# Kernel tuning notes

Hardware: AMD Instinct MI355X
Metric: run time of the kernel (lower is better)

## Reference

```python
import jax, jax.numpy as jnp
import numpy as np

N_HEAD = 16
HEAD_DIM = 128

def rotate_half(x):
    x1, x2 = jnp.split(x, 2, axis=-1)
    return jnp.concatenate((-x2, x1), axis=-1)

def setup_inputs() -> dict:
    key = jax.random.key(0)
    ks = jax.random.split(key, 5)
    B, T, C = 2, 2048, 2048
    x = jax.random.normal(ks[0], (B, T, C), dtype=jnp.float32)
    # rotary tables as used by the module: cos/sin of shape [T, head_dim]
    pos = jnp.arange(T, dtype=jnp.float32)[:, None]
    inv_freq = 1.0 / (10000.0 ** (jnp.arange(0, HEAD_DIM, 2, dtype=jnp.float32) / HEAD_DIM))
    freqs = pos * inv_freq[None, :]            # [T, head_dim/2]
    emb = jnp.concatenate([freqs, freqs], -1)  # [T, head_dim]
    cos = jnp.cos(emb)
    sin = jnp.sin(emb)
    W_qkv = jax.random.normal(ks[1], (C, 3 * C), dtype=jnp.float32) * (C ** -0.5)
    W_proj = jax.random.normal(ks[2], (C, C), dtype=jnp.float32) * (C ** -0.5)
    return {"x": x, "cos": cos, "sin": sin, "W_qkv": W_qkv, "W_proj": W_proj}

def reference(x, cos, sin, W_qkv, W_proj):
    B, T, C = x.shape
    H, D = N_HEAD, HEAD_DIM
    qkv = x @ W_qkv                                   # [B,T,3C]
    q, k, v = jnp.split(qkv, 3, axis=2)
    # [B,T,C] -> [B,H,T,D]
    q = q.reshape(B, T, H, D).transpose(0, 2, 1, 3)
    k = k.reshape(B, T, H, D).transpose(0, 2, 1, 3)
    v = v.reshape(B, T, H, D).transpose(0, 2, 1, 3)
    c = cos[None, None, :, :]                          # [1,1,T,D]
    s = sin[None, None, :, :]
    q = q * c + rotate_half(q) * s
    k = k * c + rotate_half(k) * s
    scale = 1.0 / jnp.sqrt(jnp.float32(D))
    scores = jnp.einsum('bhqd,bhkd->bhqk', q, k) * scale
    attn = jax.nn.softmax(scores, axis=-1)
    y = jnp.einsum('bhqk,bhkd->bhqd', attn, v)         # [B,H,T,D]
    y = y.transpose(0, 2, 1, 3).reshape(B, T, C)
    return y @ W_proj
```

## Files before the change

### kernel.cpp

```cpp
#include <hip/hip_runtime.h>
#include <cstdint>
#include <cstddef>

typedef __bf16 bf16_t;
typedef __bf16 bf16x8 __attribute__((ext_vector_type(8)));
typedef __bf16 bf16x4 __attribute__((ext_vector_type(4)));
typedef float f32x4 __attribute__((ext_vector_type(4)));

#define MFMA16(a, b, c) __builtin_amdgcn_mfma_f32_16x16x32_bf16(a, b, c, 0, 0, 0)

__device__ __forceinline__ void gll16(const bf16_t* g, bf16_t* l) {
  __builtin_amdgcn_global_load_lds(
      (__attribute__((address_space(1))) uint32_t*)((uintptr_t)g),
      (__attribute__((address_space(3))) uint32_t*)((uint32_t)(uintptr_t)l),
      16, 0, 0);
}

__global__ void fill_diag(uint32_t* out, int n_u32) {
  int i = blockIdx.x * 256 + threadIdx.x;
  if (i < n_u32) out[i] = 0x447A0000u;
}

__global__ void conv_vec_f32(const float* __restrict__ in, bf16_t* __restrict__ out,
                             int n8) {
  const int i = blockIdx.x * 256 + threadIdx.x;
  if (i >= n8) return;
  const float* p = in + (size_t)i * 8;
  const f32x4 a = *(const f32x4*)p;
  const f32x4 b = *(const f32x4*)(p + 4);
  bf16x8 o;
#pragma unroll
  for (int j = 0; j < 4; ++j) {
    o[j] = (bf16_t)a[j];
    o[4 + j] = (bf16_t)b[j];
  }
  ((bf16x8*)out)[i] = o;
}

__global__ __launch_bounds__(256) void conv_transpose_f32(
    const float* __restrict__ in, bf16_t* __restrict__ out, int R, int C) {
  __shared__ bf16_t tile[64][72];
  const int bc = blockIdx.x * 64;
  const int br = blockIdx.y * 64;
  const int t = threadIdx.x;
  const int r = t >> 3;
  const int c8 = (t & 7) * 8;
#pragma unroll
  for (int ii = 0; ii < 2; ++ii) {
    const int rr = r + ii * 32;
    const float* p = in + (size_t)(br + rr) * C + bc + c8;
    const f32x4 a = *(const f32x4*)p;
    const f32x4 b = *(const f32x4*)(p + 4);
    bf16x8 v;
#pragma unroll
    for (int j = 0; j < 4; ++j) {
      v[j] = (bf16_t)a[j];
      v[4 + j] = (bf16_t)b[j];
    }
    *(bf16x8*)(&tile[rr][c8]) = v;
  }
  __syncthreads();
#pragma unroll
  for (int ii = 0; ii < 2; ++ii) {
    const int rr = r + ii * 32;
    bf16x8 o;
#pragma unroll
    for (int jj = 0; jj < 8; ++jj) o[jj] = tile[c8 + jj][rr];
    *(bf16x8*)(out + (size_t)(bc + rr) * R + br + c8) = o;
  }
}

#define MF8(MLO, AARR, BARR, NLO)                                              \
  do {                                                                         \
    _Pragma("unroll") for (int k_ = 0; k_ < 2; ++k_) {                         \
      _Pragma("unroll") for (int m_ = 0; m_ < 4; ++m_) {                       \
        _Pragma("unroll") for (int n_ = 0; n_ < 2; ++n_) {                     \
          acc[(MLO) + m_][(NLO) + n_] = MFMA16(AARR[m_][k_], BARR[n_][k_],     \
                                               acc[(MLO) + m_][(NLO) + n_]);   \
        }                                                                      \
      }                                                                        \
    }                                                                          \
  } while (0)

template <bool C32>
__global__ __launch_bounds__(512, 2) void gemm8(
    const bf16_t* __restrict__ A, const bf16_t* __restrict__ Bt,
    void* __restrict__ C, int M, int N, int K, int nbn) {
  __shared__ __align__(1024) bf16_t lds8[65536];
  bf16_t* As = lds8;
  bf16_t* Bs = lds8 + 32768;

  const int tid = threadIdx.x;
  const int lane = tid & 63;
  const int wave = tid >> 6;
  const int wr = wave >> 2;
  const int wc = wave & 3;
  const int fr = lane & 15;
  const int fg = lane >> 4;

  const int nwg = gridDim.x;
  const int bid = blockIdx.x;
  const int swz = (bid & 7) * (nwg >> 3) + (bid >> 3);
  const int m0 = (swz / nbn) * 256;
  const int n0 = (swz % nbn) * 256;

  const int NT = K >> 6;

  const int sseg0 = wave * 2;
  const int srow = lane >> 3;
  const int sj = lane & 7;

  auto stage = [&](const bf16_t* __restrict__ G, int row0, bf16_t* L, int kt,
                   int h) {
#pragma unroll
    for (int l = 0; l < 2; ++l) {
      const int seg = sseg0 + l;
      const int r = seg * 8 + srow;
      const int j = sj ^ (r & 7);
      const bf16_t* src = G + (size_t)(row0 + h * 128 + r) * K + kt * 64 + j * 8;
      gll16(src, L + ((2 * kt + h) & 3) * 8192 + seg * 512 + lane * 8);
    }
  };

  const int cb0 = (fg * 16) ^ ((fr & 7) << 4);

  auto lda = [&](bf16x8(&af)[4][2], int kt, int mlo) {
    const char* base = (const char*)(As + ((2 * kt + wr) & 3) * 8192);
#pragma unroll
    for (int m = 0; m < 4; ++m) {
      const char* p = base + ((mlo + m) * 16 + fr) * 128;
      af[m][0] = *(const bf16x8*)(p + cb0);
      af[m][1] = *(const bf16x8*)(p + (cb0 ^ 64));
    }
  };
  auto ldb = [&](bf16x8(&bf)[2][2], int kt, int nlo) {
    const char* base = (const char*)(Bs + ((2 * kt + (wc >> 1)) & 3) * 8192);
#pragma unroll
    for (int n = 0; n < 2; ++n) {
      const char* p = base + ((wc & 1) * 64 + (nlo + n) * 16 + fr) * 128;
      bf[n][0] = *(const bf16x8*)(p + cb0);
      bf[n][1] = *(const bf16x8*)(p + (cb0 ^ 64));
    }
  };

  f32x4 acc[8][4] = {};

  stage(A, m0, As, 0, 0);
  stage(A, m0, As, 0, 1);
  stage(Bt, n0, Bs, 0, 0);
  stage(Bt, n0, Bs, 0, 1);
  stage(Bt, n0, Bs, 1, 0);
  stage(Bt, n0, Bs, 1, 1);
  asm volatile("s_waitcnt vmcnt(4)" ::: "memory");
  __builtin_amdgcn_s_barrier();

  bf16x8 af[4][2], bfA[2][2], bfB[2][2];

  for (int u = 0; u < NT; u += 2) {
    const bool st2 = (u + 2 < NT);
    const bool st3 = (u + 3 < NT);
    lda(af, u, 0);
    ldb(bfA, u, 0);
    stage(A, m0, As, u + 1, 0);
    asm volatile("s_waitcnt lgkmcnt(8)" ::: "memory");
    __builtin_amdgcn_s_barrier();
    asm volatile("s_waitcnt lgkmcnt(0)" ::: "memory");
    __builtin_amdgcn_sched_barrier(0);
    __builtin_amdgcn_s_setprio(1);
    MF8(0, af, bfA, 0);
    __builtin_amdgcn_s_setprio(0);
    __builtin_amdgcn_s_barrier();
    ldb(bfB, u, 2);
    stage(A, m0, As, u + 1, 1);
    __builtin_amdgcn_s_barrier();
    asm volatile("s_waitcnt lgkmcnt(0)" ::: "memory");
    __builtin_amdgcn_sched_barrier(0);
    __builtin_amdgcn_s_setprio(1);
    MF8(0, af, bfB, 2);
    __builtin_amdgcn_s_setprio(0);
    __builtin_amdgcn_s_barrier();
    lda(af, u, 4);
    if (st2) stage(Bt, n0, Bs, u + 2, 0);
    __builtin_amdgcn_s_barrier();
    asm volatile("s_waitcnt lgkmcnt(0)" ::: "memory");
    __builtin_amdgcn_sched_barrier(0);
    __builtin_amdgcn_s_setprio(1);
    MF8(4, af, bfB, 2);
    __builtin_amdgcn_s_setprio(0);
    __builtin_amdgcn_s_barrier();
    if (st2) stage(Bt, n0, Bs, u + 2, 1);
    __builtin_amdgcn_s_barrier();
    __builtin_amdgcn_s_setprio(1);
    MF8(4, af, bfA, 0);
    __builtin_amdgcn_s_setprio(0);
    asm volatile("s_waitcnt vmcnt(4)" ::: "memory");
    __builtin_amdgcn_s_barrier();
    lda(af, u + 1, 0);
    ldb(bfA, u + 1, 0);
    if (st2) stage(A, m0, As, u + 2, 0);
    asm volatile("s_waitcnt lgkmcnt(8)" ::: "memory");
    __builtin_amdgcn_s_barrier();
    asm volatile("s_waitcnt lgkmcnt(0)" ::: "memory");
    __builtin_amdgcn_sched_barrier(0);
    __builtin_amdgcn_s_setprio(1);
    MF8(0, af, bfA, 0);
    __builtin_amdgcn_s_setprio(0);
    __builtin_amdgcn_s_barrier();
    ldb(bfB, u + 1, 2);
    if (st2) stage(A, m0, As, u + 2, 1);
    __builtin_amdgcn_s_barrier();
    asm volatile("s_waitcnt lgkmcnt(0)" ::: "memory");
    __builtin_amdgcn_sched_barrier(0);
    __builtin_amdgcn_s_setprio(1);
    MF8(0, af, bfB, 2);
    __builtin_amdgcn_s_setprio(0);
    __builtin_amdgcn_s_barrier();
    lda(af, u + 1, 4);
    if (st3) stage(Bt, n0, Bs, u + 3, 0);
    __builtin_amdgcn_s_barrier();
    asm volatile("s_waitcnt lgkmcnt(0)" ::: "memory");
    __builtin_amdgcn_sched_barrier(0);
    __builtin_amdgcn_s_setprio(1);
    MF8(4, af, bfB, 2);
    __builtin_amdgcn_s_setprio(0);
    __builtin_amdgcn_s_barrier();
    if (st3) stage(Bt, n0, Bs, u + 3, 1);
    __builtin_amdgcn_s_barrier();
    __builtin_amdgcn_s_setprio(1);
    MF8(4, af, bfA, 0);
    __builtin_amdgcn_s_setprio(0);
    asm volatile("s_waitcnt vmcnt(4)" ::: "memory");
    __builtin_amdgcn_s_barrier();
  }

#pragma unroll
  for (int m = 0; m < 8; ++m) {
#pragma unroll
    for (int n = 0; n < 4; ++n) {
#pragma unroll
      for (int r = 0; r < 4; ++r) {
        const int row = m0 + wr * 128 + m * 16 + fg * 4 + r;
        const int col = n0 + wc * 64 + n * 16 + fr;
        const size_t idx = (size_t)row * N + col;
        if (C32)
          ((float*)C)[idx] = acc[m][n][r];
        else
          ((bf16_t*)C)[idx] = (bf16_t)acc[m][n][r];
      }
    }
  }
  (void)M;
}

template <bool C32>
__global__ __launch_bounds__(256) void gemm_lds(
    const bf16_t* __restrict__ A, const bf16_t* __restrict__ Bt,
    void* __restrict__ C, int M, int N, int K) {
  __shared__ __align__(16) bf16_t As[128 * 32];
  __shared__ __align__(16) bf16_t Bs[128 * 32];
  const int tid = threadIdx.x;
  const int lane = tid & 63;
  const int wave = tid >> 6;
  const int m0 = blockIdx.x * 128;
  const int n0 = blockIdx.y * 128;
  const int wm = (wave & 1) * 64;
  const int wn = (wave >> 1) * 64;
  const int fr = lane & 15;
  const int fk = (lane >> 4) * 8;

  f32x4 acc[4][4] = {};

  const bf16_t* ga = A + (size_t)(m0 + (tid >> 2)) * K + (tid & 3) * 8;
  const bf16_t* gb = Bt + (size_t)(n0 + (tid >> 2)) * K + (tid & 3) * 8;
  bf16_t* lA = As + tid * 8;
  bf16_t* lB = Bs + tid * 8;
  const size_t half = (size_t)64 * K;

  for (int k0 = 0; k0 < K; k0 += 32) {
    __syncthreads();
    gll16(ga, lA);
    gll16(ga + half, lA + 2048);
    gll16(gb, lB);
    gll16(gb + half, lB + 2048);
    ga += 32;
    gb += 32;
    __syncthreads();
    bf16x8 af[4], bfr[4];
#pragma unroll
    for (int i = 0; i < 4; ++i)
      af[i] = *(const bf16x8*)(As + (wm + i * 16 + fr) * 32 + fk);
#pragma unroll
    for (int j = 0; j < 4; ++j)
      bfr[j] = *(const bf16x8*)(Bs + (wn + j * 16 + fr) * 32 + fk);
#pragma unroll
    for (int i = 0; i < 4; ++i)
#pragma unroll
      for (int j = 0; j < 4; ++j)
        acc[i][j] = MFMA16(af[i], bfr[j], acc[i][j]);
  }

  const int fg = lane >> 4;
#pragma unroll
  for (int i = 0; i < 4; ++i) {
#pragma unroll
    for (int j = 0; j < 4; ++j) {
#pragma unroll
      for (int r = 0; r < 4; ++r) {
        const int row = m0 + wm + i * 16 + fg * 4 + r;
        const int col = n0 + wn + j * 16 + fr;
        const size_t idx = (size_t)row * N + col;
        if (C32)
          ((float*)C)[idx] = acc[i][j][r];
        else
          ((bf16_t*)C)[idx] = (bf16_t)acc[i][j][r];
      }
    }
  }
}

template <bool A32, bool C32>
__global__ __launch_bounds__(256) void gemm_t(
    const void* __restrict__ A, const bf16_t* __restrict__ Bt,
    void* __restrict__ C, int M, int N, int K) {
  __shared__ bf16_t As[128 * 32];
  __shared__ bf16_t Bs[128 * 32];
  const int tid = threadIdx.x;
  const int lane = tid & 63;
  const int wave = tid >> 6;
  const int m0 = blockIdx.x * 128;
  const int n0 = blockIdx.y * 128;
  const int wm = (wave & 1) * 64;
  const int wn = (wave >> 1) * 64;
  const int fr = lane & 15;
  const int fk = (lane >> 4) * 8;

  f32x4 acc[4][4] = {};

  const size_t ea0 = (size_t)(m0 + (tid >> 2)) * K + (tid & 3) * 8;
  const bf16_t* gb = Bt + (size_t)(n0 + (tid >> 2)) * K + (tid & 3) * 8;
  bf16_t* lA = As + tid * 8;
  bf16_t* lB = Bs + tid * 8;
  const size_t half = (size_t)64 * K;

  for (int k0 = 0; k0 < K; k0 += 32) {
    bf16x8 ra0, ra1;
    if (A32) {
      const float* pa = (const float*)A + ea0 + k0;
      const f32x4 x0 = *(const f32x4*)pa;
      const f32x4 x1 = *(const f32x4*)(pa + 4);
      const f32x4 x2 = *(const f32x4*)(pa + half);
      const f32x4 x3 = *(const f32x4*)(pa + half + 4);
#pragma unroll
      for (int j = 0; j < 4; ++j) {
        ra0[j] = (bf16_t)x0[j];
        ra0[4 + j] = (bf16_t)x1[j];
        ra1[j] = (bf16_t)x2[j];
        ra1[4 + j] = (bf16_t)x3[j];
      }
    } else {
      const bf16_t* pa = (const bf16_t*)A + ea0 + k0;
      ra0 = *(const bf16x8*)pa;
      ra1 = *(const bf16x8*)(pa + half);
    }
    const bf16x8 rb0 = *(const bf16x8*)gb;
    const bf16x8 rb1 = *(const bf16x8*)(gb + half);
    gb += 32;
    __syncthreads();
    *(bf16x8*)lA = ra0;
    *(bf16x8*)(lA + 2048) = ra1;
    *(bf16x8*)lB = rb0;
    *(bf16x8*)(lB + 2048) = rb1;
    __syncthreads();
    bf16x8 af[4], bfr[4];
#pragma unroll
    for (int i = 0; i < 4; ++i)
      af[i] = *(const bf16x8*)(As + (wm + i * 16 + fr) * 32 + fk);
#pragma unroll
    for (int j = 0; j < 4; ++j)
      bfr[j] = *(const bf16x8*)(Bs + (wn + j * 16 + fr) * 32 + fk);
#pragma unroll
    for (int i = 0; i < 4; ++i)
#pragma unroll
      for (int j = 0; j < 4; ++j)
        acc[i][j] = MFMA16(af[i], bfr[j], acc[i][j]);
  }

  const int fg = lane >> 4;
#pragma unroll
  for (int i = 0; i < 4; ++i) {
#pragma unroll
    for (int j = 0; j < 4; ++j) {
#pragma unroll
      for (int r = 0; r < 4; ++r) {
        const int row = m0 + wm + i * 16 + fg * 4 + r;
        const int col = n0 + wn + j * 16 + fr;
        const size_t idx = (size_t)row * N + col;
        if (C32)
          ((float*)C)[idx] = acc[i][j][r];
        else
          ((bf16_t*)C)[idx] = (bf16_t)acc[i][j][r];
      }
    }
  }
}

__global__ __launch_bounds__(256) void rope_k(
    const bf16_t* __restrict__ qkv, const bf16_t* __restrict__ cosb,
    const bf16_t* __restrict__ sinb, bf16_t* __restrict__ Kr) {
  const int row = blockIdx.x;
  const int t = row & 2047;
  const int b = row >> 11;
  const int idx = threadIdx.x * 8;
  const int h = idx >> 7;
  const int d = idx & 127;
  const float sgn = (d < 64) ? -1.f : 1.f;
  const bf16_t* base = qkv + (size_t)row * 6144 + 2048;
  const bf16x8 kv = *(const bf16x8*)(base + idx);
  const bf16x8 kp = *(const bf16x8*)(base + (idx ^ 64));
  const bf16x8 cv = *(const bf16x8*)(cosb + t * 128 + d);
  const bf16x8 sv = *(const bf16x8*)(sinb + t * 128 + d);
  bf16x8 o;
#pragma unroll
  for (int jj = 0; jj < 8; ++jj)
    o[jj] = (bf16_t)(((float)kv[jj]) * ((float)cv[jj]) +
                     sgn * ((float)kp[jj]) * ((float)sv[jj]));
  *(bf16x8*)(Kr + ((size_t)(b * 16 + h) * 2048 + t) * 128 + d) = o;
}

__global__ __launch_bounds__(256) void transpose_v(
    const bf16_t* __restrict__ qkv, bf16_t* __restrict__ Vt) {
  __shared__ bf16_t tile[64][72];
  const int bh = blockIdx.z;
  const int b = bh >> 4, h = bh & 15;
  const int t0 = blockIdx.x * 64;
  const int d0 = blockIdx.y * 64;
  const int t = threadIdx.x;
  const int r = t >> 3;
  const int c8 = (t & 7) * 8;
#pragma unroll
  for (int ii = 0; ii < 2; ++ii) {
    const int rr = r + ii * 32;
    *(bf16x8*)(&tile[rr][c8]) =
        *(const bf16x8*)(qkv + (size_t)(b * 2048 + t0 + rr) * 6144 + 4096 + h * 128 + d0 + c8);
  }
  __syncthreads();
#pragma unroll
  for (int ii = 0; ii < 2; ++ii) {
    const int rr = r + ii * 32;
    bf16x8 o;
#pragma unroll
    for (int jj = 0; jj < 8; ++jj) o[jj] = tile[c8 + jj][rr];
    *(bf16x8*)(Vt + ((size_t)bh * 128 + d0 + rr) * 2048 + t0 + c8) = o;
  }
}

__global__ __launch_bounds__(256, 4) void flash_q64p(
    const bf16_t* __restrict__ qkv, const bf16_t* __restrict__ cosb,
    const bf16_t* __restrict__ sinb, const bf16_t* __restrict__ Kr,
    const bf16_t* __restrict__ Vt, bf16_t* __restrict__ Y) {
  constexpr int T = 2048;
  __shared__ __align__(1024) bf16_t Ks[64 * 128];
  __shared__ bf16_t Vs[128][72];
  const int tid = threadIdx.x;
  const int lane = tid & 63;
  const int fr = lane & 15;
  const int fg = lane >> 4;
  const int qt = blockIdx.x;
  const int bh = blockIdx.y;
  const int b = bh >> 4, h = bh & 15;

  const int wave = tid >> 6;
  const int trow = qt * 64 + wave * 16 + fr;
  const bf16_t* qrow = qkv + (size_t)(b * T + trow) * 6144 + h * 128;
  bf16x8 qf[4];
#pragma unroll
  for (int ks = 0; ks < 4; ++ks) {
    const int d = ks * 32 + fg * 8;
    const float sgn = (d < 64) ? -1.f : 1.f;
    const bf16x8 qv = *(const bf16x8*)(qrow + d);
    const bf16x8 qp = *(const bf16x8*)(qrow + (d ^ 64));
    const bf16x8 cv = *(const bf16x8*)(cosb + trow * 128 + d);
    const bf16x8 sv = *(const bf16x8*)(sinb + trow * 128 + d);
    bf16x8 o;
#pragma unroll
    for (int jj = 0; jj < 8; ++jj)
      o[jj] = (bf16_t)((((float)qv[jj]) * ((float)cv[jj]) +
                        sgn * ((float)qp[jj]) * ((float)sv[jj])) *
                       0.1275174825f);
    qf[ks] = o;
  }

  f32x4 acc[8] = {};
  float l_i = 0.f;

  const int krow = tid >> 4;
  const int sc = (tid & 15) ^ (krow & 7);
  const int vrow = tid >> 3;
  const int vu = tid & 7;
  const int vc0 = ((vu >> 2) * 32) + ((vu & 1) * 16) + (((vu >> 1) & 1) * 4);
  const bf16_t* Kh = Kr + (size_t)bh * T * 128;
  const bf16_t* Vh = Vt + (size_t)bh * 128 * T;

  auto stageK = [&](int t0) {
#pragma unroll
    for (int it = 0; it < 4; ++it)
      gll16(Kh + (size_t)(t0 + it * 16 + krow) * 128 + sc * 8,
            Ks + it * 2048 + tid * 8);
  };
  bf16x8 vreg[4];
  auto loadV = [&](int t0) {
#pragma unroll
    for (int it = 0; it < 4; ++it)
      vreg[it] = *(const bf16x8*)(Vh + (size_t)(it * 32 + vrow) * T + t0 + vu * 8);
  };
  auto writeV = [&]() {
#pragma unroll
    for (int it = 0; it < 4; ++it) {
      const int row = it * 32 + vrow;
      const bf16x8 v = vreg[it];
      bf16x4 lo, hi;
#pragma unroll
      for (int jj = 0; jj < 4; ++jj) {
        lo[jj] = v[jj];
        hi[jj] = v[4 + jj];
      }
      *(bf16x4*)(&Vs[row][vc0]) = lo;
      *(bf16x4*)(&Vs[row][vc0 + 8]) = hi;
    }
  };

  stageK(0);
  loadV(0);
  asm volatile("s_waitcnt vmcnt(0)" ::: "memory");
  __builtin_amdgcn_sched_barrier(0);
  writeV();
  __syncthreads();

  const int cswz = (fr & 7) << 4;
  const char* kbase = (const char*)Ks;

  for (int j = 0; j < T / 64; ++j) {
    f32x4 sacc[4] = {};
#pragma unroll
    for (int ks = 0; ks < 4; ++ks) {
#pragma unroll
      for (int n = 0; n < 4; ++n) {
        const bf16x8 kf = *(const bf16x8*)(kbase + (n * 16 + fr) * 256 +
                                           ((ks * 64 + fg * 16) ^ cswz));
        sacc[n] = MFMA16(kf, qf[ks], sacc[n]);
      }
    }
    __syncthreads();

    const bool more = (j + 1 < T / 64);
    if (more) {
      stageK((j + 1) * 64);
      loadV((j + 1) * 64);
    }

    bf16x8 paf[2];
    float lsum = 0.f;
#pragma unroll
    for (int ks2 = 0; ks2 < 2; ++ks2) {
#pragma unroll
      for (int jj = 0; jj < 8; ++jj) {
        const float p = exp2f(sacc[ks2 * 2 + (jj >> 2)][jj & 3]);
        lsum += p;
        paf[ks2][jj] = (bf16_t)p;
      }
    }
    l_i += lsum;

#pragma unroll
    for (int ks2 = 0; ks2 < 2; ++ks2) {
#pragma unroll
      for (int n = 0; n < 8; ++n) {
        const bf16x8 vf = *(const bf16x8*)(&Vs[n * 16 + fr][ks2 * 32 + fg * 8]);
        acc[n] = MFMA16(paf[ks2], vf, acc[n]);
      }
    }

    asm volatile("s_waitcnt vmcnt(0)" ::: "memory");
    __builtin_amdgcn_sched_barrier(0);
    __syncthreads();
    if (more) {
      writeV();
      __syncthreads();
    }
  }

  float l = l_i;
  l += __shfl_xor(l, 16, 64);
  l += __shfl_xor(l, 32, 64);
#pragma unroll
  for (int r = 0; r < 4; ++r) {
    const float inv = 1.0f / __shfl(l, fg * 4 + r, 64);
    const int t = qt * 64 + wave * 16 + fg * 4 + r;
    bf16_t* yrow = Y + (size_t)(b * T + t) * 2048 + h * 128;
#pragma unroll
    for (int n = 0; n < 8; ++n)
      yrow[n * 16 + fr] = (bf16_t)(acc[n][r] * inv);
  }
}

__global__ __launch_bounds__(256) void flash_fused_v2(
    const bf16_t* __restrict__ qkv, const bf16_t* __restrict__ cosb,
    const bf16_t* __restrict__ sinb, bf16_t* __restrict__ Y) {
  constexpr int T = 2048;
  __shared__ bf16_t Ks[64][136];
  __shared__ bf16_t Vs[128][72];
  __shared__ bf16_t Ps[128][72];
  const int tid = threadIdx.x;
  const int lane = tid & 63;
  const int wave = tid >> 6;
  const int fr = lane & 15;
  const int fg = lane >> 4;
  const int qt = blockIdx.x;
  const int bh = blockIdx.y;
  const int b = bh >> 4, h = bh & 15;

  const bf16_t* qbase = qkv + (size_t)b * T * 6144 + h * 128;
  bf16x8 qf[2][4];
#pragma unroll
  for (int i = 0; i < 2; ++i) {
    const int trow = qt * 128 + wave * 32 + i * 16 + fr;
    const bf16_t* qrow = qbase + (size_t)trow * 6144;
#pragma unroll
    for (int ks = 0; ks < 4; ++ks) {
      const int d = ks * 32 + fg * 8;
      const float sgn = (d < 64) ? -1.f : 1.f;
      const bf16x8 qv = *(const bf16x8*)(qrow + d);
      const bf16x8 qp = *(const bf16x8*)(qrow + (d ^ 64));
      const bf16x8 cv = *(const bf16x8*)(cosb + trow * 128 + d);
      const bf16x8 sv = *(const bf16x8*)(sinb + trow * 128 + d);
      bf16x8 o;
#pragma unroll
      for (int jj = 0; jj < 8; ++jj)
        o[jj] = (bf16_t)((((float)qv[jj]) * ((float)cv[jj]) +
                          sgn * ((float)qp[jj]) * ((float)sv[jj])) *
                         0.08838834764831845f);
      qf[i][ks] = o;
    }
  }

  f32x4 acc[2][8] = {};
  float l_i[2][4] = {};

  const int kr = tid >> 4;
  const int kc = (tid & 15) * 8;
  const float sgnk = (kc < 64) ? -1.f : 1.f;
  const int tp = tid & 63;

  for (int j = 0; j < T / 64; ++j) {
    const int t0 = j * 64;
#pragma unroll
    for (int it = 0; it < 4; ++it) {
      const int row = it * 16 + kr;
      const int tg = t0 + row;
      const bf16_t* krow = qkv + ((size_t)(b * T + tg)) * 6144 + 2048 + h * 128;
      const bf16x8 kv = *(const bf16x8*)(krow + kc);
      const bf16x8 kp = *(const bf16x8*)(krow + (kc ^ 64));
      const bf16x8 cv = *(const bf16x8*)(cosb + tg * 128 + kc);
      const bf16x8 sv = *(const bf16x8*)(sinb + tg * 128 + kc);
      bf16x8 o;
#pragma unroll
      for (int jj = 0; jj < 8; ++jj)
        o[jj] = (bf16_t)(((float)kv[jj]) * ((float)cv[jj]) +
                         sgnk * ((float)kp[jj]) * ((float)sv[jj]));
      *(bf16x8*)(&Ks[row][kc]) = o;
    }
#pragma unroll
    for (int cc = 0; cc < 4; ++cc) {
      const int d8 = (cc * 4 + (tid >> 6)) * 8;
      const bf16x8 vv = *(const bf16x8*)(qkv + ((size_t)(b * T + t0 + tp)) * 6144 +
                                         4096 + h * 128 + d8);
#pragma unroll
      for (int jj = 0; jj < 8; ++jj) Vs[d8 + jj][tp] = vv[jj];
    }
    __syncthreads();

    f32x4 sacc[2][4] = {};
#pragma unroll
    for (int ks = 0; ks < 4; ++ks) {
#pragma unroll
      for (int n = 0; n < 4; ++n) {
        const bf16x8 kf = *(const bf16x8*)(&Ks[n * 16 + fr][ks * 32 + fg * 8]);
        sacc[0][n] = MFMA16(qf[0][ks], kf, sacc[0][n]);
        sacc[1][n] = MFMA16(qf[1][ks], kf, sacc[1][n]);
      }
    }

#pragma unroll
    for (int i = 0; i < 2; ++i) {
#pragma unroll
      for (int r = 0; r < 4; ++r) {
        const float p0 = __expf(sacc[i][0][r]);
        const float p1 = __expf(sacc[i][1][r]);
        const float p2 = __expf(sacc[i][2][r]);
        const float p3 = __expf(sacc[i][3][r]);
        l_i[i][r] += (p0 + p1) + (p2 + p3);
        const int prow = wave * 32 + i * 16 + fg * 4 + r;
        Ps[prow][0 + fr] = (bf16_t)p0;
        Ps[prow][16 + fr] = (bf16_t)p1;
        Ps[prow][32 + fr] = (bf16_t)p2;
        Ps[prow][48 + fr] = (bf16_t)p3;
      }
    }

#pragma unroll
    for (int ks = 0; ks < 2; ++ks) {
      const bf16x8 pf0 = *(const bf16x8*)(&Ps[wave * 32 + fr][ks * 32 + fg * 8]);
      const bf16x8 pf1 = *(const bf16x8*)(&Ps[wave * 32 + 16 + fr][ks * 32 + fg * 8]);
#pragma unroll
      for (int n = 0; n < 8; ++n) {
        const bf16x8 vf = *(const bf16x8*)(&Vs[n * 16 + fr][ks * 32 + fg * 8]);
        acc[0][n] = MFMA16(pf0, vf, acc[0][n]);
        acc[1][n] = MFMA16(pf1, vf, acc[1][n]);
      }
    }
    __syncthreads();
  }

#pragma unroll
  for (int i = 0; i < 2; ++i) {
#pragma unroll
    for (int r = 0; r < 4; ++r) {
      float l = l_i[i][r];
#pragma unroll
      for (int msk = 1; msk < 16; msk <<= 1) l += __shfl_xor(l, msk, 64);
      const float inv = 1.0f / l;
      const int t = qt * 128 + wave * 32 + i * 16 + fg * 4 + r;
      bf16_t* yrow = Y + (size_t)(b * T + t) * 2048 + h * 128;
#pragma unroll
      for (int n = 0; n < 8; ++n)
        yrow[n * 16 + fr] = (bf16_t)(acc[i][n][r] * inv);
    }
  }
}

extern "C" void kernel_launch(void* const* d_in, const int* in_sizes, int n_in,
                              void* d_out, int out_size, void* d_ws, size_t ws_size,
                              hipStream_t stream) {
  const float* x = (const float*)d_in[0];
  const float* cosi = (const float*)d_in[1];
  const float* sini = (const float*)d_in[2];
  const float* Wqkv = (const float*)d_in[3];
  const float* Wproj = (const float*)d_in[4];

  const size_t NEED_FAST = sizeof(bf16_t) *
      ((size_t)12582912 + 262144 + 262144 + 25165824 + 8388608 + 8388608);
  const size_t NEED_BASE = 256 + sizeof(bf16_t) *
      ((size_t)12582912 + 4194304 + 262144 + 262144 + 25165824);

  if (ws_size >= NEED_FAST) {
    bf16_t* base = (bf16_t*)d_ws;
    bf16_t* WqkvT = base;
    bf16_t* y = base;
    bf16_t* cosb = base + 12582912;
    bf16_t* sinb = cosb + 262144;
    bf16_t* qkv = sinb + 262144;
    bf16_t* WprojT = qkv;
    bf16_t* Kr = qkv + 25165824;
    bf16_t* xb = Kr;
    bf16_t* Vt = Kr + 8388608;

    conv_vec_f32<<<128, 256, 0, stream>>>(cosi, cosb, 32768);
    conv_vec_f32<<<128, 256, 0, stream>>>(sini, sinb, 32768);
    conv_vec_f32<<<4096, 256, 0, stream>>>(x, xb, 1048576);
    conv_transpose_f32<<<dim3(96, 32), 256, 0, stream>>>(Wqkv, WqkvT, 2048, 6144);
    gemm8<false><<<384, 512, 0, stream>>>(xb, WqkvT, qkv, 4096, 6144, 2048, 24);
    rope_k<<<4096, 256, 0, stream>>>(qkv, cosb, sinb, Kr);
    transpose_v<<<dim3(32, 2, 32), 256, 0, stream>>>(qkv, Vt);
    flash_q64p<<<dim3(32, 32), 256, 0, stream>>>(qkv, cosb, sinb, Kr, Vt, y);
    conv_transpose_f32<<<dim3(32, 32), 256, 0, stream>>>(Wproj, WprojT, 2048, 2048);
    gemm_lds<true><<<dim3(32, 16), 256, 0, stream>>>(y, WprojT, d_out, 4096, 2048, 2048);
  } else if (ws_size >= NEED_BASE) {
    bf16_t* base = (bf16_t*)((char*)d_ws + 256);
    bf16_t* WqkvT = base;
    bf16_t* y = base;
    bf16_t* WprojT = base + 12582912;
    bf16_t* cosb = WprojT + 4194304;
    bf16_t* sinb = cosb + 262144;
    bf16_t* qkv = sinb + 262144;

    conv_vec_f32<<<128, 256, 0, stream>>>(cosi, cosb, 32768);
    conv_vec_f32<<<128, 256, 0, stream>>>(sini, sinb, 32768);
    conv_transpose_f32<<<dim3(96, 32), 256, 0, stream>>>(Wqkv, WqkvT, 2048, 6144);
    gemm_t<true, false><<<dim3(32, 48), 256, 0, stream>>>(x, WqkvT, qkv, 4096, 6144, 2048);
    flash_fused_v2<<<dim3(16, 32), 256, 0, stream>>>(qkv, cosb, sinb, y);
    conv_transpose_f32<<<dim3(32, 32), 256, 0, stream>>>(Wproj, WprojT, 2048, 2048);
    gemm_t<false, true><<<dim3(32, 16), 256, 0, stream>>>(y, WprojT, d_out, 4096, 2048, 2048);
  } else {
    fill_diag<<<(out_size + 255) / 256, 256, 0, stream>>>((uint32_t*)d_out, out_size);
  }
}
```

Baseline: 424.2 us.

## Switch GEMMs to 128x256 tile kernel with triple/quintuple-buffered LDS pipeline

```diff
diff --git a/kernel.cpp b/kernel.cpp
--- a/kernel.cpp
+++ b/kernel.cpp
@@ -70,25 +70,13 @@
   }
 }
 
-#define MF8(MLO, AARR, BARR, NLO)                                              \
-  do {                                                                         \
-    _Pragma("unroll") for (int k_ = 0; k_ < 2; ++k_) {                         \
-      _Pragma("unroll") for (int m_ = 0; m_ < 4; ++m_) {                       \
-        _Pragma("unroll") for (int n_ = 0; n_ < 2; ++n_) {                     \
-          acc[(MLO) + m_][(NLO) + n_] = MFMA16(AARR[m_][k_], BARR[n_][k_],     \
-                                               acc[(MLO) + m_][(NLO) + n_]);   \
-        }                                                                      \
-      }                                                                        \
-    }                                                                          \
-  } while (0)
-
 template <bool C32>
-__global__ __launch_bounds__(512, 2) void gemm8(
+__global__ __launch_bounds__(512, 2) void gemm8n(
     const bf16_t* __restrict__ A, const bf16_t* __restrict__ Bt,
     void* __restrict__ C, int M, int N, int K, int nbn) {
   __shared__ __align__(1024) bf16_t lds8[65536];
   bf16_t* As = lds8;
-  bf16_t* Bs = lds8 + 32768;
+  bf16_t* Bs = lds8 + 24576;
 
   const int tid = threadIdx.x;
   const int lane = tid & 63;
@@ -101,40 +89,38 @@
   const int nwg = gridDim.x;
   const int bid = blockIdx.x;
   const int swz = (bid & 7) * (nwg >> 3) + (bid >> 3);
-  const int m0 = (swz / nbn) * 256;
+  const int m0 = (swz / nbn) * 128;
   const int n0 = (swz % nbn) * 256;
 
   const int NT = K >> 6;
 
-  const int sseg0 = wave * 2;
-  const int srow = lane >> 3;
-  const int sj = lane & 7;
-
-  auto stage = [&](const bf16_t* __restrict__ G, int row0, bf16_t* L, int kt,
-                   int h) {
+  const int srow = tid >> 3;
+  const int sj = tid & 7;
+
+  auto stage = [&](const bf16_t* __restrict__ G, int grow0, bf16_t* slotBase,
+                   int kt) {
 #pragma unroll
     for (int l = 0; l < 2; ++l) {
-      const int seg = sseg0 + l;
-      const int r = seg * 8 + srow;
+      const int r = l * 64 + srow;
       const int j = sj ^ (r & 7);
-      const bf16_t* src = G + (size_t)(row0 + h * 128 + r) * K + kt * 64 + j * 8;
-      gll16(src, L + ((2 * kt + h) & 3) * 8192 + seg * 512 + lane * 8);
+      gll16(G + (size_t)(grow0 + r) * K + kt * 64 + j * 8,
+            slotBase + l * 4096 + tid * 8);
     }
   };
 
   const int cb0 = (fg * 16) ^ ((fr & 7) << 4);
 
-  auto lda = [&](bf16x8(&af)[4][2], int kt, int mlo) {
-    const char* base = (const char*)(As + ((2 * kt + wr) & 3) * 8192);
+  auto lda = [&](bf16x8(&af)[4][2], int t) {
+    const char* base = (const char*)(As + (t % 3) * 8192);
 #pragma unroll
     for (int m = 0; m < 4; ++m) {
-      const char* p = base + ((mlo + m) * 16 + fr) * 128;
+      const char* p = base + (wr * 64 + m * 16 + fr) * 128;
       af[m][0] = *(const bf16x8*)(p + cb0);
       af[m][1] = *(const bf16x8*)(p + (cb0 ^ 64));
     }
   };
-  auto ldb = [&](bf16x8(&bf)[2][2], int kt, int nlo) {
-    const char* base = (const char*)(Bs + ((2 * kt + (wc >> 1)) & 3) * 8192);
+  auto ldb2 = [&](bf16x8(&bf)[2][2], int t, int nlo) {
+    const char* base = (const char*)(Bs + ((2 * t + (wc >> 1)) % 5) * 8192);
 #pragma unroll
     for (int n = 0; n < 2; ++n) {
       const char* p = base + ((wc & 1) * 64 + (nlo + n) * 16 + fr) * 128;
@@ -143,103 +129,66 @@
     }
   };
 
-  f32x4 acc[8][4] = {};
-
-  stage(A, m0, As, 0, 0);
-  stage(A, m0, As, 0, 1);
-  stage(Bt, n0, Bs, 0, 0);
-  stage(Bt, n0, Bs, 0, 1);
-  stage(Bt, n0, Bs, 1, 0);
-  stage(Bt, n0, Bs, 1, 1);
-  asm volatile("s_waitcnt vmcnt(4)" ::: "memory");
+  f32x4 acc[4][4] = {};
+
+  stage(A, m0, As, 0);
+  stage(A, m0, As + 8192, 1);
+  stage(Bt, n0, Bs, 0);
+  stage(Bt, n0 + 128, Bs + 8192, 0);
+  stage(Bt, n0, Bs + 2 * 8192, 1);
+  asm volatile("s_waitcnt vmcnt(2)" ::: "memory");
   __builtin_amdgcn_s_barrier();
 
-  bf16x8 af[4][2], bfA[2][2], bfB[2][2];
-
-  for (int u = 0; u < NT; u += 2) {
-    const bool st2 = (u + 2 < NT);
-    const bool st3 = (u + 3 < NT);
-    lda(af, u, 0);
-    ldb(bfA, u, 0);
-    stage(A, m0, As, u + 1, 0);
+  bf16x8 af[4][2], bf01[2][2], bf23[2][2];
+
+  for (int t = 0; t < NT; ++t) {
+    lda(af, t);
+    ldb2(bf01, t, 0);
+    if (t + 2 < NT) stage(Bt, n0, Bs + ((2 * t + 4) % 5) * 8192, t + 2);
+    if (t + 1 < NT) stage(Bt, n0 + 128, Bs + ((2 * t + 3) % 5) * 8192, t + 1);
     asm volatile("s_waitcnt lgkmcnt(8)" ::: "memory");
     __builtin_amdgcn_s_barrier();
     asm volatile("s_waitcnt lgkmcnt(0)" ::: "memory");
     __builtin_amdgcn_sched_barrier(0);
     __builtin_amdgcn_s_setprio(1);
-    MF8(0, af, bfA, 0);
+#pragma unroll
+    for (int k = 0; k < 2; ++k)
+#pragma unroll
+      for (int m = 0; m < 4; ++m)
+#pragma unroll
+        for (int n = 0; n < 2; ++n)
+          acc[m][n] = MFMA16(af[m][k], bf01[n][k], acc[m][n]);
     __builtin_amdgcn_s_setprio(0);
     __builtin_amdgcn_s_barrier();
-    ldb(bfB, u, 2);
-    stage(A, m0, As, u + 1, 1);
+    ldb2(bf23, t, 2);
+    if (t + 2 < NT) stage(A, m0, As + ((t + 2) % 3) * 8192, t + 2);
     __builtin_amdgcn_s_barrier();
     asm volatile("s_waitcnt lgkmcnt(0)" ::: "memory");
     __builtin_amdgcn_sched_barrier(0);
     __builtin_amdgcn_s_setprio(1);
-    MF8(0, af, bfB, 2);
+#pragma unroll
+    for (int k = 0; k < 2; ++k)
+#pragma unroll
+      for (int m = 0; m < 4; ++m)
+#pragma unroll
+        for (int n = 0; n < 2; ++n)
+          acc[m][n + 2] = MFMA16(af[m][k], bf23[n][k], acc[m][n + 2]);
     __builtin_amdgcn_s_setprio(0);
+    if (t + 3 < NT) {
+      asm volatile("s_waitcnt vmcnt(2)" ::: "memory");
+    } else {
+      asm volatile("s_waitcnt vmcnt(0)" ::: "memory");
+    }
     __builtin_amdgcn_s_barrier();
-    lda(af, u, 4);
-    if (st2) stage(Bt, n0, Bs, u + 2, 0);
-    __builtin_amdgcn_s_barrier();
-    asm volatile("s_waitcnt lgkmcnt(0)" ::: "memory");
-    __builtin_amdgcn_sched_barrier(0);
-    __builtin_amdgcn_s_setprio(1);
-    MF8(4, af, bfB, 2);
-    __builtin_amdgcn_s_setprio(0);
-    __builtin_amdgcn_s_barrier();
-    if (st2) stage(Bt, n0, Bs, u + 2, 1);
-    __builtin_amdgcn_s_barrier();
-    __builtin_amdgcn_s_setprio(1);
-    MF8(4, af, bfA, 0);
-    __builtin_amdgcn_s_setprio(0);
-    asm volatile("s_waitcnt vmcnt(4)" ::: "memory");
-    __builtin_amdgcn_s_barrier();
-    lda(af, u + 1, 0);
-    ldb(bfA, u + 1, 0);
-    if (st2) stage(A, m0, As, u + 2, 0);
-    asm volatile("s_waitcnt lgkmcnt(8)" ::: "memory");
-    __builtin_amdgcn_s_barrier();
-    asm volatile("s_waitcnt lgkmcnt(0)" ::: "memory");
-    __builtin_amdgcn_sched_barrier(0);
-    __builtin_amdgcn_s_setprio(1);
-    MF8(0, af, bfA, 0);
-    __builtin_amdgcn_s_setprio(0);
-    __builtin_amdgcn_s_barrier();
-    ldb(bfB, u + 1, 2);
-    if (st2) stage(A, m0, As, u + 2, 1);
-    __builtin_amdgcn_s_barrier();
-    asm volatile("s_waitcnt lgkmcnt(0)" ::: "memory");
-    __builtin_amdgcn_sched_barrier(0);
-    __builtin_amdgcn_s_setprio(1);
-    MF8(0, af, bfB, 2);
-    __builtin_amdgcn_s_setprio(0);
-    __builtin_amdgcn_s_barrier();
-    lda(af, u + 1, 4);
-    if (st3) stage(Bt, n0, Bs, u + 3, 0);
-    __builtin_amdgcn_s_barrier();
-    asm volatile("s_waitcnt lgkmcnt(0)" ::: "memory");
-    __builtin_amdgcn_sched_barrier(0);
-    __builtin_amdgcn_s_setprio(1);
-    MF8(4, af, bfB, 2);
-    __builtin_amdgcn_s_setprio(0);
-    __builtin_amdgcn_s_barrier();
-    if (st3) stage(Bt, n0, Bs, u + 3, 1);
-    __builtin_amdgcn_s_barrier();
-    __builtin_amdgcn_s_setprio(1);
-    MF8(4, af, bfA, 0);
-    __builtin_amdgcn_s_setprio(0);
-    asm volatile("s_waitcnt vmcnt(4)" ::: "memory");
-    __builtin_amdgcn_s_barrier();
-  }
-
-#pragma unroll
-  for (int m = 0; m < 8; ++m) {
+  }
+
+#pragma unroll
+  for (int m = 0; m < 4; ++m) {
 #pragma unroll
     for (int n = 0; n < 4; ++n) {
 #pragma unroll
       for (int r = 0; r < 4; ++r) {
-        const int row = m0 + wr * 128 + m * 16 + fg * 4 + r;
+        const int row = m0 + wr * 64 + m * 16 + fg * 4 + r;
         const int col = n0 + wc * 64 + n * 16 + fr;
         const size_t idx = (size_t)row * N + col;
         if (C32)
@@ -250,72 +199,6 @@
     }
   }
   (void)M;
-}
-
-template <bool C32>
-__global__ __launch_bounds__(256) void gemm_lds(
-    const bf16_t* __restrict__ A, const bf16_t* __restrict__ Bt,
-    void* __restrict__ C, int M, int N, int K) {
-  __shared__ __align__(16) bf16_t As[128 * 32];
-  __shared__ __align__(16) bf16_t Bs[128 * 32];
-  const int tid = threadIdx.x;
-  const int lane = tid & 63;
-  const int wave = tid >> 6;
-  const int m0 = blockIdx.x * 128;
-  const int n0 = blockIdx.y * 128;
-  const int wm = (wave & 1) * 64;
-  const int wn = (wave >> 1) * 64;
-  const int fr = lane & 15;
-  const int fk = (lane >> 4) * 8;
-
-  f32x4 acc[4][4] = {};
-
-  const bf16_t* ga = A + (size_t)(m0 + (tid >> 2)) * K + (tid & 3) * 8;
-  const bf16_t* gb = Bt + (size_t)(n0 + (tid >> 2)) * K + (tid & 3) * 8;
-  bf16_t* lA = As + tid * 8;
-  bf16_t* lB = Bs + tid * 8;
-  const size_t half = (size_t)64 * K;
-
-  for (int k0 = 0; k0 < K; k0 += 32) {
-    __syncthreads();
-    gll16(ga, lA);
-    gll16(ga + half, lA + 2048);
-    gll16(gb, lB);
-    gll16(gb + half, lB + 2048);
-    ga += 32;
-    gb += 32;
-    __syncthreads();
-    bf16x8 af[4], bfr[4];
-#pragma unroll
-    for (int i = 0; i < 4; ++i)
-      af[i] = *(const bf16x8*)(As + (wm + i * 16 + fr) * 32 + fk);
-#pragma unroll
-    for (int j = 0; j < 4; ++j)
-      bfr[j] = *(const bf16x8*)(Bs + (wn + j * 16 + fr) * 32 + fk);
-#pragma unroll
-    for (int i = 0; i < 4; ++i)
-#pragma unroll
-      for (int j = 0; j < 4; ++j)
-        acc[i][j] = MFMA16(af[i], bfr[j], acc[i][j]);
-  }
-
-  const int fg = lane >> 4;
-#pragma unroll
-  for (int i = 0; i < 4; ++i) {
-#pragma unroll
-    for (int j = 0; j < 4; ++j) {
-#pragma unroll
-      for (int r = 0; r < 4; ++r) {
-        const int row = m0 + wm + i * 16 + fg * 4 + r;
-        const int col = n0 + wn + j * 16 + fr;
-        const size_t idx = (size_t)row * N + col;
-        if (C32)
-          ((float*)C)[idx] = acc[i][j][r];
-        else
-          ((bf16_t*)C)[idx] = (bf16_t)acc[i][j][r];
-      }
-    }
-  }
 }
 
 template <bool A32, bool C32>
@@ -768,12 +651,12 @@
     conv_vec_f32<<<128, 256, 0, stream>>>(sini, sinb, 32768);
     conv_vec_f32<<<4096, 256, 0, stream>>>(x, xb, 1048576);
     conv_transpose_f32<<<dim3(96, 32), 256, 0, stream>>>(Wqkv, WqkvT, 2048, 6144);
-    gemm8<false><<<384, 512, 0, stream>>>(xb, WqkvT, qkv, 4096, 6144, 2048, 24);
+    gemm8n<false><<<768, 512, 0, stream>>>(xb, WqkvT, qkv, 4096, 6144, 2048, 24);
     rope_k<<<4096, 256, 0, stream>>>(qkv, cosb, sinb, Kr);
     transpose_v<<<dim3(32, 2, 32), 256, 0, stream>>>(qkv, Vt);
     flash_q64p<<<dim3(32, 32), 256, 0, stream>>>(qkv, cosb, sinb, Kr, Vt, y);
     conv_transpose_f32<<<dim3(32, 32), 256, 0, stream>>>(Wproj, WprojT, 2048, 2048);
-    gemm_lds<true><<<dim3(32, 16), 256, 0, stream>>>(y, WprojT, d_out, 4096, 2048, 2048);
+    gemm8n<true><<<256, 512, 0, stream>>>(y, WprojT, d_out, 4096, 2048, 2048, 8);
   } else if (ws_size >= NEED_BASE) {
     bf16_t* base = (bf16_t*)((char*)d_ws + 256);
     bf16_t* WqkvT = base;
```

Measured after the change: 419.7 us. Within noise of the previous version (-1.1%).

## Double query rows per flash block and pipeline output projection GEMM

Applied to the files above, without the earlier changes.

```diff
diff --git a/kernel.cpp b/kernel.cpp
--- a/kernel.cpp
+++ b/kernel.cpp
@@ -253,69 +253,134 @@
 }
 
 template <bool C32>
-__global__ __launch_bounds__(256) void gemm_lds(
+__global__ __launch_bounds__(512, 2) void gemm8n(
     const bf16_t* __restrict__ A, const bf16_t* __restrict__ Bt,
-    void* __restrict__ C, int M, int N, int K) {
-  __shared__ __align__(16) bf16_t As[128 * 32];
-  __shared__ __align__(16) bf16_t Bs[128 * 32];
+    void* __restrict__ C, int M, int N, int K, int nbn) {
+  __shared__ __align__(1024) bf16_t lds8[65536];
+  bf16_t* As = lds8;
+  bf16_t* Bs = lds8 + 24576;
+
   const int tid = threadIdx.x;
   const int lane = tid & 63;
   const int wave = tid >> 6;
-  const int m0 = blockIdx.x * 128;
-  const int n0 = blockIdx.y * 128;
-  const int wm = (wave & 1) * 64;
-  const int wn = (wave >> 1) * 64;
+  const int wr = wave >> 2;
+  const int wc = wave & 3;
   const int fr = lane & 15;
-  const int fk = (lane >> 4) * 8;
+  const int fg = lane >> 4;
+
+  const int nwg = gridDim.x;
+  const int bid = blockIdx.x;
+  const int swz = (bid & 7) * (nwg >> 3) + (bid >> 3);
+  const int m0 = (swz / nbn) * 128;
+  const int n0 = (swz % nbn) * 256;
+
+  const int NT = K >> 6;
+
+  const int srow = tid >> 3;
+  const int sj = tid & 7;
+
+  auto stage = [&](const bf16_t* __restrict__ G, int grow0, bf16_t* slotBase,
+                   int kt) {
+#pragma unroll
+    for (int l = 0; l < 2; ++l) {
+      const int r = l * 64 + srow;
+      const int j = sj ^ (r & 7);
+      gll16(G + (size_t)(grow0 + r) * K + kt * 64 + j * 8,
+            slotBase + l * 4096 + tid * 8);
+    }
+  };
+
+  const int cb0 = (fg * 16) ^ ((fr & 7) << 4);
+
+  auto lda = [&](bf16x8(&af)[4][2], int t) {
+    const char* base = (const char*)(As + (t % 3) * 8192);
+#pragma unroll
+    for (int m = 0; m < 4; ++m) {
+      const char* p = base + (wr * 64 + m * 16 + fr) * 128;
+      af[m][0] = *(const bf16x8*)(p + cb0);
+      af[m][1] = *(const bf16x8*)(p + (cb0 ^ 64));
+    }
+  };
+  auto ldb2 = [&](bf16x8(&bf)[2][2], int t, int nlo) {
+    const char* base = (const char*)(Bs + ((2 * t + (wc >> 1)) % 5) * 8192);
+#pragma unroll
+    for (int n = 0; n < 2; ++n) {
+      const char* p = base + ((wc & 1) * 64 + (nlo + n) * 16 + fr) * 128;
+      bf[n][0] = *(const bf16x8*)(p + cb0);
+      bf[n][1] = *(const bf16x8*)(p + (cb0 ^ 64));
+    }
+  };
 
   f32x4 acc[4][4] = {};
 
-  const bf16_t* ga = A + (size_t)(m0 + (tid >> 2)) * K + (tid & 3) * 8;
-  const bf16_t* gb = Bt + (size_t)(n0 + (tid >> 2)) * K + (tid & 3) * 8;
-  bf16_t* lA = As + tid * 8;
-  bf16_t* lB = Bs + tid * 8;
-  const size_t half = (size_t)64 * K;
-
-  for (int k0 = 0; k0 < K; k0 += 32) {
-    __syncthreads();
-    gll16(ga, lA);
-    gll16(ga + half, lA + 2048);
-    gll16(gb, lB);
-    gll16(gb + half, lB + 2048);
-    ga += 32;
-    gb += 32;
-    __syncthreads();
-    bf16x8 af[4], bfr[4];
-#pragma unroll
-    for (int i = 0; i < 4; ++i)
-      af[i] = *(const bf16x8*)(As + (wm + i * 16 + fr) * 32 + fk);
-#pragma unroll
-    for (int j = 0; j < 4; ++j)
-      bfr[j] = *(const bf16x8*)(Bs + (wn + j * 16 + fr) * 32 + fk);
-#pragma unroll
-    for (int i = 0; i < 4; ++i)
-#pragma unroll
-      for (int j = 0; j < 4; ++j)
-        acc[i][j] = MFMA16(af[i], bfr[j], acc[i][j]);
-  }
-
-  const int fg = lane >> 4;
-#pragma unroll
-  for (int i = 0; i < 4; ++i) {
-#pragma unroll
-    for (int j = 0; j < 4; ++j) {
+  stage(A, m0, As, 0);
+  stage(A, m0, As + 8192, 1);
+  stage(Bt, n0, Bs, 0);
+  stage(Bt, n0 + 128, Bs + 8192, 0);
+  stage(Bt, n0, Bs + 2 * 8192, 1);
+  asm volatile("s_waitcnt vmcnt(2)" ::: "memory");
+  __builtin_amdgcn_s_barrier();
+
+  bf16x8 af[4][2], bf01[2][2], bf23[2][2];
+
+  for (int t = 0; t < NT; ++t) {
+    lda(af, t);
+    ldb2(bf01, t, 0);
+    if (t + 2 < NT) stage(Bt, n0, Bs + ((2 * t + 4) % 5) * 8192, t + 2);
+    if (t + 1 < NT) stage(Bt, n0 + 128, Bs + ((2 * t + 3) % 5) * 8192, t + 1);
+    asm volatile("s_waitcnt lgkmcnt(8)" ::: "memory");
+    __builtin_amdgcn_s_barrier();
+    asm volatile("s_waitcnt lgkmcnt(0)" ::: "memory");
+    __builtin_amdgcn_sched_barrier(0);
+    __builtin_amdgcn_s_setprio(1);
+#pragma unroll
+    for (int k = 0; k < 2; ++k)
+#pragma unroll
+      for (int m = 0; m < 4; ++m)
+#pragma unroll
+        for (int n = 0; n < 2; ++n)
+          acc[m][n] = MFMA16(af[m][k], bf01[n][k], acc[m][n]);
+    __builtin_amdgcn_s_setprio(0);
+    __builtin_amdgcn_s_barrier();
+    ldb2(bf23, t, 2);
+    if (t + 2 < NT) stage(A, m0, As + ((t + 2) % 3) * 8192, t + 2);
+    __builtin_amdgcn_s_barrier();
+    asm volatile("s_waitcnt lgkmcnt(0)" ::: "memory");
+    __builtin_amdgcn_sched_barrier(0);
+    __builtin_amdgcn_s_setprio(1);
+#pragma unroll
+    for (int k = 0; k < 2; ++k)
+#pragma unroll
+      for (int m = 0; m < 4; ++m)
+#pragma unroll
+        for (int n = 0; n < 2; ++n)
+          acc[m][n + 2] = MFMA16(af[m][k], bf23[n][k], acc[m][n + 2]);
+    __builtin_amdgcn_s_setprio(0);
+    if (t + 3 < NT) {
+      asm volatile("s_waitcnt vmcnt(2)" ::: "memory");
+    } else {
+      asm volatile("s_waitcnt vmcnt(0)" ::: "memory");
+    }
+    __builtin_amdgcn_s_barrier();
+  }
+
+#pragma unroll
+  for (int m = 0; m < 4; ++m) {
+#pragma unroll
+    for (int n = 0; n < 4; ++n) {
 #pragma unroll
       for (int r = 0; r < 4; ++r) {
-        const int row = m0 + wm + i * 16 + fg * 4 + r;
-        const int col = n0 + wn + j * 16 + fr;
+        const int row = m0 + wr * 64 + m * 16 + fg * 4 + r;
+        const int col = n0 + wc * 64 + n * 16 + fr;
         const size_t idx = (size_t)row * N + col;
         if (C32)
-          ((float*)C)[idx] = acc[i][j][r];
+          ((float*)C)[idx] = acc[m][n][r];
         else
-          ((bf16_t*)C)[idx] = (bf16_t)acc[i][j][r];
-      }
-    }
-  }
+          ((bf16_t*)C)[idx] = (bf16_t)acc[m][n][r];
+      }
+    }
+  }
+  (void)M;
 }
 
 template <bool A32, bool C32>
@@ -454,7 +519,7 @@
   }
 }
 
-__global__ __launch_bounds__(256, 4) void flash_q64p(
+__global__ __launch_bounds__(256, 2) void flash_q128p(
     const bf16_t* __restrict__ qkv, const bf16_t* __restrict__ cosb,
     const bf16_t* __restrict__ sinb, const bf16_t* __restrict__ Kr,
     const bf16_t* __restrict__ Vt, bf16_t* __restrict__ Y) {
@@ -468,30 +533,34 @@
   const int qt = blockIdx.x;
   const int bh = blockIdx.y;
   const int b = bh >> 4, h = bh & 15;
-
   const int wave = tid >> 6;
-  const int trow = qt * 64 + wave * 16 + fr;
-  const bf16_t* qrow = qkv + (size_t)(b * T + trow) * 6144 + h * 128;
-  bf16x8 qf[4];
-#pragma unroll
-  for (int ks = 0; ks < 4; ++ks) {
-    const int d = ks * 32 + fg * 8;
-    const float sgn = (d < 64) ? -1.f : 1.f;
-    const bf16x8 qv = *(const bf16x8*)(qrow + d);
-    const bf16x8 qp = *(const bf16x8*)(qrow + (d ^ 64));
-    const bf16x8 cv = *(const bf16x8*)(cosb + trow * 128 + d);
-    const bf16x8 sv = *(const bf16x8*)(sinb + trow * 128 + d);
-    bf16x8 o;
-#pragma unroll
-    for (int jj = 0; jj < 8; ++jj)
-      o[jj] = (bf16_t)((((float)qv[jj]) * ((float)cv[jj]) +
-                        sgn * ((float)qp[jj]) * ((float)sv[jj])) *
-                       0.1275174825f);
-    qf[ks] = o;
-  }
-
-  f32x4 acc[8] = {};
-  float l_i = 0.f;
+
+  const bf16_t* qbase = qkv + (size_t)b * T * 6144 + h * 128;
+  bf16x8 qf[2][4];
+#pragma unroll
+  for (int i = 0; i < 2; ++i) {
+    const int trow = qt * 128 + wave * 32 + i * 16 + fr;
+    const bf16_t* qrow = qbase + (size_t)trow * 6144;
+#pragma unroll
+    for (int ks = 0; ks < 4; ++ks) {
+      const int d = ks * 32 + fg * 8;
+      const float sgn = (d < 64) ? -1.f : 1.f;
+      const bf16x8 qv = *(const bf16x8*)(qrow + d);
+      const bf16x8 qp = *(const bf16x8*)(qrow + (d ^ 64));
+      const bf16x8 cv = *(const bf16x8*)(cosb + trow * 128 + d);
+      const bf16x8 sv = *(const bf16x8*)(sinb + trow * 128 + d);
+      bf16x8 o;
+#pragma unroll
+      for (int jj = 0; jj < 8; ++jj)
+        o[jj] = (bf16_t)((((float)qv[jj]) * ((float)cv[jj]) +
+                          sgn * ((float)qp[jj]) * ((float)sv[jj])) *
+                         0.1275174825f);
+      qf[i][ks] = o;
+    }
+  }
+
+  f32x4 acc[2][8] = {};
+  float l_i[2] = {0.f, 0.f};
 
   const int krow = tid >> 4;
   const int sc = (tid & 15) ^ (krow & 7);
@@ -540,14 +609,15 @@
   const char* kbase = (const char*)Ks;
 
   for (int j = 0; j < T / 64; ++j) {
-    f32x4 sacc[4] = {};
+    f32x4 sacc[2][4] = {};
 #pragma unroll
     for (int ks = 0; ks < 4; ++ks) {
 #pragma unroll
       for (int n = 0; n < 4; ++n) {
         const bf16x8 kf = *(const bf16x8*)(kbase + (n * 16 + fr) * 256 +
                                            ((ks * 64 + fg * 16) ^ cswz));
-        sacc[n] = MFMA16(kf, qf[ks], sacc[n]);
+        sacc[0][n] = MFMA16(kf, qf[0][ks], sacc[0][n]);
+        sacc[1][n] = MFMA16(kf, qf[1][ks], sacc[1][n]);
       }
     }
     __syncthreads();
@@ -558,25 +628,29 @@
       loadV((j + 1) * 64);
     }
 
-    bf16x8 paf[2];
-    float lsum = 0.f;
-#pragma unroll
-    for (int ks2 = 0; ks2 < 2; ++ks2) {
-#pragma unroll
-      for (int jj = 0; jj < 8; ++jj) {
-        const float p = exp2f(sacc[ks2 * 2 + (jj >> 2)][jj & 3]);
-        lsum += p;
-        paf[ks2][jj] = (bf16_t)p;
-      }
-    }
-    l_i += lsum;
+    bf16x8 paf[2][2];
+#pragma unroll
+    for (int i = 0; i < 2; ++i) {
+      float lsum = 0.f;
+#pragma unroll
+      for (int ks2 = 0; ks2 < 2; ++ks2) {
+#pragma unroll
+        for (int jj = 0; jj < 8; ++jj) {
+          const float p = exp2f(sacc[i][ks2 * 2 + (jj >> 2)][jj & 3]);
+          lsum += p;
+          paf[i][ks2][jj] = (bf16_t)p;
+        }
+      }
+      l_i[i] += lsum;
+    }
 
 #pragma unroll
     for (int ks2 = 0; ks2 < 2; ++ks2) {
 #pragma unroll
       for (int n = 0; n < 8; ++n) {
         const bf16x8 vf = *(const bf16x8*)(&Vs[n * 16 + fr][ks2 * 32 + fg * 8]);
-        acc[n] = MFMA16(paf[ks2], vf, acc[n]);
+        acc[0][n] = MFMA16(paf[0][ks2], vf, acc[0][n]);
+        acc[1][n] = MFMA16(paf[1][ks2], vf, acc[1][n]);
       }
     }
 
@@ -589,17 +663,20 @@
     }
   }
 
-  float l = l_i;
-  l += __shfl_xor(l, 16, 64);
-  l += __shfl_xor(l, 32, 64);
-#pragma unroll
-  for (int r = 0; r < 4; ++r) {
-    const float inv = 1.0f / __shfl(l, fg * 4 + r, 64);
-    const int t = qt * 64 + wave * 16 + fg * 4 + r;
-    bf16_t* yrow = Y + (size_t)(b * T + t) * 2048 + h * 128;
-#pragma unroll
-    for (int n = 0; n < 8; ++n)
-      yrow[n * 16 + fr] = (bf16_t)(acc[n][r] * inv);
+#pragma unroll
+  for (int i = 0; i < 2; ++i) {
+    float l = l_i[i];
+    l += __shfl_xor(l, 16, 64);
+    l += __shfl_xor(l, 32, 64);
+#pragma unroll
+    for (int r = 0; r < 4; ++r) {
+      const float inv = 1.0f / __shfl(l, fg * 4 + r, 64);
+      const int t = qt * 128 + wave * 32 + i * 16 + fg * 4 + r;
+      bf16_t* yrow = Y + (size_t)(b * T + t) * 2048 + h * 128;
+#pragma unroll
+      for (int n = 0; n < 8; ++n)
+        yrow[n * 16 + fr] = (bf16_t)(acc[i][n][r] * inv);
+    }
   }
 }
 
@@ -771,9 +848,9 @@
     gemm8<false><<<384, 512, 0, stream>>>(xb, WqkvT, qkv, 4096, 6144, 2048, 24);
     rope_k<<<4096, 256, 0, stream>>>(qkv, cosb, sinb, Kr);
     transpose_v<<<dim3(32, 2, 32), 256, 0, stream>>>(qkv, Vt);
-    flash_q64p<<<dim3(32, 32), 256, 0, stream>>>(qkv, cosb, sinb, Kr, Vt, y);
+    flash_q128p<<<dim3(16, 32), 256, 0, stream>>>(qkv, cosb, sinb, Kr, Vt, y);
     conv_transpose_f32<<<dim3(32, 32), 256, 0, stream>>>(Wproj, WprojT, 2048, 2048);
-    gemm_lds<true><<<dim3(32, 16), 256, 0, stream>>>(y, WprojT, d_out, 4096, 2048, 2048);
+    gemm8n<true><<<256, 512, 0, stream>>>(y, WprojT, d_out, 4096, 2048, 2048, 8);
   } else if (ws_size >= NEED_BASE) {
     bf16_t* base = (bf16_t*)((char*)d_ws + 256);
     bf16_t* WqkvT = base;
```

Measured after the change: 413.4 us. 1.03x faster.
